# Kernel optimization log

Hardware: AMD Instinct MI355X
Metric: run time of the kernel (lower is better)

Reference implementation:

```python
import jax, jax.numpy as jnp
import numpy as np

EPS = 1e-8


def setup_inputs() -> dict:
    key = jax.random.key(0)
    k1, k2, k3, k4 = jax.random.split(key, 4)
    N, Cin, Cout, S, DHW, K = 4, 64, 64, 512, 48, 3
    return {
        "x": jax.random.normal(k1, (N, Cin, DHW, DHW, DHW), dtype=jnp.float32),
        "s": jax.random.normal(k2, (N, S), dtype=jnp.float32),
        "style_weight": jax.random.normal(k3, (Cin, S), dtype=jnp.float32) * (1.0 / np.sqrt(S)),
        "style_bias": jnp.ones((Cin,), dtype=jnp.float32),
        "weight": jax.random.normal(k4, (Cout, Cin, K, K, K), dtype=jnp.float32) * (1.0 / np.sqrt(Cin * K**3)),
        "bias": jnp.zeros((Cout,), dtype=jnp.float32),
    }


def reference(x, s, style_weight, style_bias, weight, bias):
    N, Cin = x.shape[0], x.shape[1]
    Cout = weight.shape[0]
    # style modulation: per-sample per-input-channel scale
    style = s @ style_weight.T + style_bias                      # [N, Cin]
    w = weight[None] * style[:, None, :, None, None, None]       # [N, Cout, Cin, k, k, k]
    # demodulation over fan-in dims (Cin, k, k, k)
    w = w * jax.lax.rsqrt(jnp.sum(w * w, axis=(2, 3, 4, 5), keepdims=True) + EPS)
    w = w.reshape(N * Cout, Cin, *w.shape[3:])                   # grouped kernel
    xg = x.reshape(1, N * Cin, *x.shape[2:])
    y = jax.lax.conv_general_dilated(
        xg, w,
        window_strides=(1, 1, 1),
        padding='VALID',
        feature_group_count=N,
        dimension_numbers=('NCDHW', 'OIDHW', 'NCDHW'),
    )                                                            # [1, N*Cout, D', H', W']
    y = y.reshape(N, Cout, *y.shape[2:])
    return y + bias[None, :, None, None, None]
```

## Files before the change

kernel.cpp:

```cpp
#include <hip/hip_runtime.h>

typedef float f32x4 __attribute__((ext_vector_type(4)));
typedef short bf16x8 __attribute__((ext_vector_type(8)));

#define AS1 __attribute__((address_space(1)))
#define AS3 __attribute__((address_space(3)))

__device__ __forceinline__ void gl16(const void* g, void* l) {
  __builtin_amdgcn_global_load_lds((const AS1 unsigned int*)g,
                                   (AS3 unsigned int*)l, 16, 0, 0);
}

__device__ __forceinline__ unsigned short f2bf(float f) {
  unsigned u = __float_as_uint(f);
  u = u + 0x7FFFu + ((u >> 16) & 1u);
  return (unsigned short)(u >> 16);
}

__global__ __launch_bounds__(256) void k_wmod(const float* __restrict__ s,
                                              const float* __restrict__ sw,
                                              const float* __restrict__ sb,
                                              const float* __restrict__ weight,
                                              unsigned short* __restrict__ wm) {
  int o = blockIdx.x, n = blockIdx.y, t = threadIdx.x;
  int lane = t & 63, wv = t >> 6;
  __shared__ float st4[64][5];
  __shared__ float st[64];
  {
    int i = t >> 2, part = t & 3;
    const float4* swp = (const float4*)(sw + i * 512 + part * 128);
    const float4* sp4 = (const float4*)(s + n * 512 + part * 128);
    float a = 0.f;
#pragma unroll 8
    for (int kk = 0; kk < 32; ++kk) {
      float4 w4 = swp[kk], s4 = sp4[kk];
      a += w4.x * s4.x + w4.y * s4.y + w4.z * s4.z + w4.w * s4.w;
    }
    st4[i][part] = a;
  }
  __syncthreads();
  if (t < 64) st[t] = st4[t][0] + st4[t][1] + st4[t][2] + st4[t][3] + sb[t];
  __syncthreads();

  const float* wp = weight + o * 1728;
  float v[7];
  float ss = 0.f;
#pragma unroll
  for (int j = 0; j < 7; ++j) {
    int idx = t + j * 256;
    float w = 0.f;
    if (idx < 1728) {
      int i = idx / 27;
      w = wp[idx] * st[i];
    }
    v[j] = w;
    ss += w * w;
  }
#pragma unroll
  for (int off = 32; off > 0; off >>= 1) ss += __shfl_down(ss, off);
  __shared__ float red[4];
  if (lane == 0) red[wv] = ss;
  __syncthreads();
  float total = red[0] + red[1] + red[2] + red[3];
  float dm = 1.0f / sqrtf(total + 1e-8f);
#pragma unroll
  for (int j = 0; j < 7; ++j) {
    int idx = t + j * 256;
    if (idx < 1728) {
      int i = idx / 27, k = idx - i * 27;
      int g = (n * 27 + k) * 64 + o;
      wm[g * 64 + (((i >> 3) ^ (o & 7)) << 3) + (i & 7)] = f2bf(v[j] * dm);
    }
  }
}

__global__ __launch_bounds__(256) void k_xpose(const float* __restrict__ x,
                                               unsigned short* __restrict__ xT) {
  __shared__ unsigned tile[256][33];
  int n = blockIdx.y;
  int p0 = blockIdx.x * 256;
  int t = threadIdx.x;
  int wv = t >> 6, lane = t & 63;
  const float* xb = x + (size_t)n * 64 * 110592 + p0 + 4 * lane;
#pragma unroll
  for (int c = 0; c < 8; ++c) {
    int i2 = wv + 4 * c;
    const float4 a = *(const float4*)(xb + (size_t)(2 * i2) * 110592);
    const float4 b = *(const float4*)(xb + (size_t)(2 * i2 + 1) * 110592);
    tile[4 * lane + 0][i2] = (unsigned)f2bf(a.x) | ((unsigned)f2bf(b.x) << 16);
    tile[4 * lane + 1][i2] = (unsigned)f2bf(a.y) | ((unsigned)f2bf(b.y) << 16);
    tile[4 * lane + 2][i2] = (unsigned)f2bf(a.z) | ((unsigned)f2bf(b.z) << 16);
    tile[4 * lane + 3][i2] = (unsigned)f2bf(a.w) | ((unsigned)f2bf(b.w) << 16);
  }
  __syncthreads();
  uint4* dst = (uint4*)xT;
  int sl = t & 7;
#pragma unroll
  for (int pass = 0; pass < 8; ++pass) {
    int p = (t >> 3) + 32 * pass;
    int c = sl ^ (p & 7);
    uint4 u;
    u.x = tile[p][4 * c + 0];
    u.y = tile[p][4 * c + 1];
    u.z = tile[p][4 * c + 2];
    u.w = tile[p][4 * c + 3];
    dst[(size_t)(n * 110592 + p0 + p) * 8 + sl] = u;
  }
}

__global__ __launch_bounds__(256) void k_conv(const unsigned short* __restrict__ xT,
                                              const unsigned short* __restrict__ wm,
                                              const float* __restrict__ bias,
                                              float* __restrict__ out) {
  __shared__ uint4 Bl4[37888 / 16];
  __shared__ uint4 Al4[2][8192 / 16];
  char* Bl = (char*)Bl4;

  int bid = blockIdx.x;
  int orig = (bid & 7) * 276 + (bid >> 3);
  int n = orig / 552;
  int pb = orig - n * 552;
  int p0 = pb * 192;

  int t = threadIdx.x;
  int lane = t & 63, wv = t >> 6;
  int l15 = lane & 15, lhi = lane >> 4;
  f32x4 acc[4][3] = {};

  const char* xb = (const char*)xT + ((size_t)(n * 110592 + p0)) * 128;
  const char* wb = (const char*)wm + (size_t)n * 27 * 8192;

  int aoff[8];
#pragma unroll
  for (int m = 0; m < 4; ++m)
#pragma unroll
    for (int ih = 0; ih < 2; ++ih) {
      int orow = m * 16 + l15;
      int c = lhi + ih * 4;
      aoff[m * 2 + ih] = orow * 128 + ((c ^ (orow & 7)) << 4);
    }

  {
    gl16(wb + wv * 1024 + lane * 16, (char*)Al4[0] + wv * 1024);
    gl16(wb + (wv + 4) * 1024 + lane * 16, (char*)Al4[0] + (wv + 4) * 1024);
  }

#pragma unroll
  for (int kd = 0; kd < 3; ++kd) {
    const char* src = xb + (size_t)kd * (2304 * 128);
    for (int cc = wv; cc < 37; cc += 4)
      gl16(src + cc * 1024 + lane * 16, Bl + cc * 1024);
    asm volatile("s_waitcnt vmcnt(0)" ::: "memory");
    __builtin_amdgcn_s_barrier();
    __builtin_amdgcn_sched_barrier(0);

#pragma unroll
    for (int tap = 0; tap < 9; ++tap) {
      const int s = kd * 9 + tap;
      const int cur = s & 1;
      if (s + 1 < 27) {
        const char* ap = wb + (size_t)(s + 1) * 8192;
        gl16(ap + wv * 1024 + lane * 16, (char*)Al4[cur ^ 1] + wv * 1024);
        gl16(ap + (wv + 4) * 1024 + lane * 16, (char*)Al4[cur ^ 1] + (wv + 4) * 1024);
      }
      const int kh = tap / 3, kw = tap - kh * 3;
      const int rbase = wv * 48 + kh * 48 + kw;
      const char* Alc = (const char*)Al4[cur];
#pragma unroll
      for (int ih = 0; ih < 2; ++ih) {
        int c = lhi + ih * 4;
        bf16x8 a[4], b[3];
#pragma unroll
        for (int m = 0; m < 4; ++m)
          a[m] = *(const bf16x8*)(Alc + aoff[m * 2 + ih]);
#pragma unroll
        for (int q = 0; q < 3; ++q) {
          int r = rbase + q * 16 + l15;
          b[q] = *(const bf16x8*)(Bl + r * 128 + ((c ^ (r & 7)) << 4));
        }
        __builtin_amdgcn_s_setprio(1);
#pragma unroll
        for (int m = 0; m < 4; ++m)
#pragma unroll
          for (int q = 0; q < 3; ++q)
            acc[m][q] = __builtin_amdgcn_mfma_f32_16x16x32_bf16(a[m], b[q], acc[m][q], 0, 0, 0);
        __builtin_amdgcn_s_setprio(0);
      }
      asm volatile("s_waitcnt vmcnt(0)" ::: "memory");
      __builtin_amdgcn_s_barrier();
      __builtin_amdgcn_sched_barrier(0);
    }
  }

  float bv[4][4];
#pragma unroll
  for (int m = 0; m < 4; ++m)
#pragma unroll
    for (int r = 0; r < 4; ++r) bv[m][r] = bias[m * 16 + lhi * 4 + r];

  float* ob = out + (size_t)n * 64 * 97336;
#pragma unroll
  for (int q = 0; q < 3; ++q) {
    int p = p0 + wv * 48 + q * 16 + l15;
    int d = p / 2304;
    int rem = p - d * 2304;
    int h = rem / 48;
    int w = rem - h * 48;
    if (h < 46 && w < 46) {
      int base = d * 2116 + h * 46 + w;
#pragma unroll
      for (int m = 0; m < 4; ++m)
#pragma unroll
        for (int r = 0; r < 4; ++r) {
          int o = m * 16 + lhi * 4 + r;
          ob[(size_t)o * 97336 + base] = acc[m][q][r] + bv[m][r];
        }
    }
  }
}

extern "C" void kernel_launch(void* const* d_in, const int* in_sizes, int n_in,
                              void* d_out, int out_size, void* d_ws, size_t ws_size,
                              hipStream_t stream) {
  const float* x    = (const float*)d_in[0];
  const float* s    = (const float*)d_in[1];
  const float* sw   = (const float*)d_in[2];
  const float* sb   = (const float*)d_in[3];
  const float* wt   = (const float*)d_in[4];
  const float* bias = (const float*)d_in[5];
  float* out = (float*)d_out;

  unsigned short* wm    = (unsigned short*)((char*)d_ws + 1024);
  unsigned short* xT    = (unsigned short*)((char*)d_ws + 1024 + 884736);

  hipLaunchKernelGGL(k_wmod, dim3(64, 4), dim3(256), 0, stream, s, sw, sb, wt, wm);
  hipLaunchKernelGGL(k_xpose, dim3(432, 4), dim3(256), 0, stream, x, xT);
  hipLaunchKernelGGL(k_conv, dim3(2208), dim3(256), 0, stream, xT, wm, bias, out);
}
```

Baseline: 151.1 us.

## Enlarge conv tiles to 512 threads and stage all nine taps per depth slice

The conv kernel doubles the block to 8 waves covering 384 output positions. For each kd slice it loads the input slab and all nine tap weight tiles into LDS in one go. This drops the per-tap double-buffered weight prefetch and its 27 barriers, leaving three barrier phases and spreading each weight load over twice as many positions. The cost is about 136KB of LDS per block, so only one block fits per CU, and global loads no longer overlap with the MFMA work.

```diff
diff --git a/kernel.cpp b/kernel.cpp
--- a/kernel.cpp
+++ b/kernel.cpp
@@ -108,19 +108,20 @@
   }
 }
 
-__global__ __launch_bounds__(256) void k_conv(const unsigned short* __restrict__ xT,
-                                              const unsigned short* __restrict__ wm,
-                                              const float* __restrict__ bias,
-                                              float* __restrict__ out) {
-  __shared__ uint4 Bl4[37888 / 16];
-  __shared__ uint4 Al4[2][8192 / 16];
+__global__ __launch_bounds__(512, 2) void k_conv(const unsigned short* __restrict__ xT,
+                                                 const unsigned short* __restrict__ wm,
+                                                 const float* __restrict__ bias,
+                                                 float* __restrict__ out) {
+  __shared__ uint4 Bl4[62464 / 16];
+  __shared__ uint4 Al4[73728 / 16];
   char* Bl = (char*)Bl4;
+  char* Al = (char*)Al4;
 
   int bid = blockIdx.x;
-  int orig = (bid & 7) * 276 + (bid >> 3);
-  int n = orig / 552;
-  int pb = orig - n * 552;
-  int p0 = pb * 192;
+  int orig = (bid & 7) * 138 + (bid >> 3);
+  int n = orig / 276;
+  int pb = orig - n * 276;
+  int p0 = pb * 384;
 
   int t = threadIdx.x;
   int lane = t & 63, wv = t >> 6;
@@ -140,39 +141,31 @@
       aoff[m * 2 + ih] = orow * 128 + ((c ^ (orow & 7)) << 4);
     }
 
-  {
-    gl16(wb + wv * 1024 + lane * 16, (char*)Al4[0] + wv * 1024);
-    gl16(wb + (wv + 4) * 1024 + lane * 16, (char*)Al4[0] + (wv + 4) * 1024);
-  }
-
 #pragma unroll
   for (int kd = 0; kd < 3; ++kd) {
+    if (kd) __builtin_amdgcn_s_barrier();
     const char* src = xb + (size_t)kd * (2304 * 128);
-    for (int cc = wv; cc < 37; cc += 4)
+    for (int cc = wv; cc < 61; cc += 8)
       gl16(src + cc * 1024 + lane * 16, Bl + cc * 1024);
+    const char* asrc = wb + (size_t)kd * 73728;
+    for (int cc = wv; cc < 72; cc += 8)
+      gl16(asrc + cc * 1024 + lane * 16, Al + cc * 1024);
     asm volatile("s_waitcnt vmcnt(0)" ::: "memory");
     __builtin_amdgcn_s_barrier();
     __builtin_amdgcn_sched_barrier(0);
 
 #pragma unroll
-    for (int tap = 0; tap < 9; ++tap) {
-      const int s = kd * 9 + tap;
-      const int cur = s & 1;
-      if (s + 1 < 27) {
-        const char* ap = wb + (size_t)(s + 1) * 8192;
-        gl16(ap + wv * 1024 + lane * 16, (char*)Al4[cur ^ 1] + wv * 1024);
-        gl16(ap + (wv + 4) * 1024 + lane * 16, (char*)Al4[cur ^ 1] + (wv + 4) * 1024);
-      }
-      const int kh = tap / 3, kw = tap - kh * 3;
+    for (int tp = 0; tp < 9; ++tp) {
+      const int kh = tp / 3, kw = tp % 3;
       const int rbase = wv * 48 + kh * 48 + kw;
-      const char* Alc = (const char*)Al4[cur];
+      const char* At = Al + tp * 8192;
 #pragma unroll
       for (int ih = 0; ih < 2; ++ih) {
         int c = lhi + ih * 4;
         bf16x8 a[4], b[3];
 #pragma unroll
         for (int m = 0; m < 4; ++m)
-          a[m] = *(const bf16x8*)(Alc + aoff[m * 2 + ih]);
+          a[m] = *(const bf16x8*)(At + aoff[m * 2 + ih]);
 #pragma unroll
         for (int q = 0; q < 3; ++q) {
           int r = rbase + q * 16 + l15;
@@ -186,9 +179,6 @@
             acc[m][q] = __builtin_amdgcn_mfma_f32_16x16x32_bf16(a[m], b[q], acc[m][q], 0, 0, 0);
         __builtin_amdgcn_s_setprio(0);
       }
-      asm volatile("s_waitcnt vmcnt(0)" ::: "memory");
-      __builtin_amdgcn_s_barrier();
-      __builtin_amdgcn_sched_barrier(0);
     }
   }
 
@@ -235,5 +225,5 @@
 
   hipLaunchKernelGGL(k_wmod, dim3(64, 4), dim3(256), 0, stream, s, sw, sb, wt, wm);
   hipLaunchKernelGGL(k_xpose, dim3(432, 4), dim3(256), 0, stream, x, xT);
-  hipLaunchKernelGGL(k_conv, dim3(2208), dim3(256), 0, stream, xT, wm, bias, out);
-}
+  hipLaunchKernelGGL(k_conv, dim3(1104), dim3(512), 0, stream, xT, wm, bias, out);
+}
```

Measured after the change: 146.9 us. 1.03x faster.
